# Kernel tuning notes

Hardware: AMD Instinct MI355X
Metric: run time of the kernel (lower is better)

The kernel has to match this reference:

```python
import jax, jax.numpy as jnp
import numpy as np

# ---- static config (mirrors init_kwargs and the chosen batch geometry) ----
HID = 4096; NH = 32; NKV = 8; HD = HID // NH; GRP = NH // NKV
PAGE = 16; MAXP = 2048; B = 4; QLEN = 512; PREV = 1016
THETA = 10000.0
PREV_PAGES = (PREV + PAGE - 1) // PAGE              # 64 pages already in cache per request
LAST_LEN = PREV - (PREV_PAGES - 1) * PAGE           # 8 valid slots in last cached page
NEW_PAGES = (QLEN + LAST_LEN + PAGE - 1) // PAGE - 1  # 32 pages allocated per request
TOT_PAGES = PREV_PAGES + NEW_PAGES                   # 96
KV_LEN = TOT_PAGES * PAGE                            # 1536 (padded)
TOT = PREV + QLEN                                    # 1528 valid kv tokens


def setup_inputs() -> dict:
    key = jax.random.key(0)
    ks = jax.random.split(key, 6)
    hidden_states = jax.random.normal(ks[0], (B, QLEN, HID), jnp.float32)
    paged_kv_data = jax.random.normal(ks[1], (MAXP, 2, PAGE, NKV, HD), jnp.float32)
    Wq = jax.random.normal(ks[2], (HID, HID), jnp.float32) * 0.02
    Wk = jax.random.normal(ks[3], (NKV * HD, HID), jnp.float32) * 0.02
    Wv = jax.random.normal(ks[4], (NKV * HD, HID), jnp.float32) * 0.02
    Wo = jax.random.normal(ks[5], (HID, HID), jnp.float32) * 0.02
    qo_indptr = jnp.arange(B + 1, dtype=jnp.int32) * QLEN
    paged_kv_indptr = jnp.arange(B + 1, dtype=jnp.int32) * PREV_PAGES
    paged_kv_indices = jnp.arange(B * PREV_PAGES, dtype=jnp.int32)  # pages 0..255 in use
    paged_kv_last_page_len = jnp.full((B,), LAST_LEN, jnp.int32)
    return dict(hidden_states=hidden_states, paged_kv_data=paged_kv_data,
                Wq=Wq, Wk=Wk, Wv=Wv, Wo=Wo, qo_indptr=qo_indptr,
                paged_kv_indptr=paged_kv_indptr, paged_kv_indices=paged_kv_indices,
                paged_kv_last_page_len=paged_kv_last_page_len)


def _rope(x, pos):
    # x: [B, L, H, D], pos: [L]; Llama rotate-half RoPE (flashinfer ROPE_LLAMA)
    d = x.shape[-1]; d2 = d // 2
    inv = 1.0 / (THETA ** (jnp.arange(0, d, 2, dtype=jnp.float32) / d))
    ang = pos[:, None] * inv                     # [L, d/2]
    cos = jnp.cos(ang)[None, :, None, :]
    sin = jnp.sin(ang)[None, :, None, :]
    x1, x2 = x[..., :d2], x[..., d2:]
    return jnp.concatenate([x1 * cos - x2 * sin, x2 * cos + x1 * sin], axis=-1)


def reference(hidden_states, paged_kv_data, Wq, Wk, Wv, Wo, qo_indptr,
              paged_kv_indptr, paged_kv_indices, paged_kv_last_page_len):
    q = (hidden_states @ Wq.T).reshape(B, QLEN, NH, HD)
    k = (hidden_states @ Wk.T).reshape(B, QLEN, NKV, HD)
    v = (hidden_states @ Wv.T).reshape(B, QLEN, NKV, HD)

    # ---- paged KV-cache append (vectorized form of update_kv_cache) ----
    # free pages in ascending id order, as in the torch mask/arange logic
    used = jnp.zeros((MAXP,), bool).at[paged_kv_indices].set(True)
    avail = jnp.sort(jnp.where(used, MAXP, jnp.arange(MAXP)))[: B * NEW_PAGES].astype(jnp.int32)
    new_pages = avail.reshape(B, NEW_PAGES)               # sequential per-request allocation
    last_page = paged_kv_indices[paged_kv_indptr[1:] - 1]  # [B] partially-filled last page
    append_pages = jnp.concatenate([last_page[:, None], new_pages], axis=1)  # [B, NEW_PAGES+1]
    t = LAST_LEN + jnp.arange(QLEN)                       # slot offset within the append window
    slot = t % PAGE                                       # [QLEN]
    dest_page = append_pages[:, t // PAGE]                # [B, QLEN]
    paged_kv_data = paged_kv_data.at[dest_page, 0, slot[None, :]].set(k)
    paged_kv_data = paged_kv_data.at[dest_page, 1, slot[None, :]].set(v)

    new_indices2d = jnp.concatenate([paged_kv_indices.reshape(B, PREV_PAGES), new_pages], axis=1)
    new_indptr = jnp.arange(B + 1, dtype=jnp.int32) * TOT_PAGES
    new_last = jnp.full((B,), (LAST_LEN + QLEN - 1) % PAGE + 1, jnp.int32)

    # ---- batched prefill attention over paged cache, RoPE applied on the fly ----
    K = paged_kv_data[new_indices2d, 0].reshape(B, KV_LEN, NKV, HD)
    V = paged_kv_data[new_indices2d, 1].reshape(B, KV_LEN, NKV, HD)
    kpos = jnp.arange(KV_LEN, dtype=jnp.float32)
    qpos = jnp.arange(PREV, PREV + QLEN, dtype=jnp.float32)
    qr = _rope(q, qpos)
    Kr = _rope(K, kpos)
    Kg = jnp.repeat(Kr, GRP, axis=2)   # GQA: each kv head serves GRP query heads
    Vg = jnp.repeat(V, GRP, axis=2)
    scores = jnp.einsum('bqhd,bkhd->bhqk', qr, Kg) * (HD ** -0.5)
    mask = (kpos[None, :] <= qpos[:, None]) & (kpos[None, :] < TOT)  # causal + padded-slot mask
    scores = jnp.where(mask[None, None], scores, jnp.float32(-1e30))
    attn = jax.nn.softmax(scores, axis=-1)
    out = jnp.einsum('bhqk,bkhd->bqhd', attn, Vg).reshape(B, QLEN, HID)
    out = out @ Wo.T
    return out, paged_kv_data, new_indptr, new_indices2d.reshape(-1), new_last
```

## Files before the change

### kernel.cpp

```cpp
#include <hip/hip_runtime.h>
#include <stdint.h>

#define B_ 4
#define QLEN_ 512
#define HID_ 4096
#define NH_ 32
#define NKV_ 8
#define HD_ 128
#define PREV_ 1016
#define TOTLEN_ 1528
#define KVLEN_ 1536
#define PREV_PAGES_ 64
#define NEW_PAGES_ 32
#define TOT_PAGES_ 96
#define MAXP_ 2048

typedef unsigned short u16;
typedef __attribute__((ext_vector_type(8))) short short8;
typedef __attribute__((ext_vector_type(4))) float f32x4;

__device__ __forceinline__ u16 f2bf(float x) {
  unsigned u = __float_as_uint(x);
  u += 0x7fffu + ((u >> 16) & 1u);
  return (u16)(u >> 16);
}

__global__ void conv_bf16(const float* __restrict__ in, u16* __restrict__ out, int n8) {
  int i = blockIdx.x * 256 + threadIdx.x;
  if (i >= n8) return;
  size_t base = (size_t)i * 8;
  float4 a = *(const float4*)(in + base);
  float4 b = *(const float4*)(in + base + 4);
  union { u16 u[8]; short8 v; } r;
  r.u[0] = f2bf(a.x); r.u[1] = f2bf(a.y); r.u[2] = f2bf(a.z); r.u[3] = f2bf(a.w);
  r.u[4] = f2bf(b.x); r.u[5] = f2bf(b.y); r.u[6] = f2bf(b.z); r.u[7] = f2bf(b.w);
  *(short8*)(out + base) = r.v;
}

__global__ void page_setup(const int* __restrict__ kv_indptr, const int* __restrict__ kv_indices,
                           float* __restrict__ out_ints, int* __restrict__ aps) {
  __shared__ unsigned char used[MAXP_];
  __shared__ int offs[256];
  __shared__ int avail[B_ * NEW_PAGES_];
  int tid = threadIdx.x;
  for (int j = tid; j < MAXP_; j += 256) used[j] = 0;
  __syncthreads();
  for (int j = tid; j < B_ * PREV_PAGES_; j += 256) used[kv_indices[j]] = 1;
  __syncthreads();
  int cnt = 0;
  for (int i = 0; i < 8; i++) cnt += 1 - (int)used[tid * 8 + i];
  offs[tid] = cnt;
  __syncthreads();
  if (tid == 0) {
    int run = 0;
    for (int i = 0; i < 256; i++) { int c = offs[i]; offs[i] = run; run += c; }
  }
  __syncthreads();
  int run = offs[tid];
  for (int i = 0; i < 8; i++) {
    int p = tid * 8 + i;
    if (!used[p]) { if (run < B_ * NEW_PAGES_) avail[run] = p; run++; }
  }
  __syncthreads();
  if (tid < B_ + 1) out_ints[tid] = (float)(tid * TOT_PAGES_);
  if (tid < B_) out_ints[B_ + 1 + B_ * TOT_PAGES_ + tid] = 8.0f;
  for (int j = tid; j < B_ * TOT_PAGES_; j += 256) {
    int b = j / TOT_PAGES_, r = j % TOT_PAGES_;
    int v = (r < PREV_PAGES_) ? kv_indices[b * PREV_PAGES_ + r] : avail[b * NEW_PAGES_ + (r - PREV_PAGES_)];
    out_ints[B_ + 1 + j] = (float)v;
  }
  for (int j = tid; j < B_ * 33; j += 256) {
    int b = j / 33, r = j % 33;
    aps[j] = (r == 0) ? kv_indices[kv_indptr[b + 1] - 1] : avail[b * NEW_PAGES_ + r - 1];
  }
}

__device__ __forceinline__ void async16(const u16* g, u16* l) {
  __builtin_amdgcn_global_load_lds((const __attribute__((address_space(1))) unsigned int*)g,
                                   (__attribute__((address_space(3))) unsigned int*)l, 16, 0, 0);
}

__global__ __launch_bounds__(256) void gemm_bt(const u16* __restrict__ A, const u16* __restrict__ Bm,
                                               float* __restrict__ C, int M, int N, int K) {
  __shared__ u16 a_sm[4096];
  __shared__ u16 b_sm[4096];
  const int tid = threadIdx.x;
  const int wave = tid >> 6, lane = tid & 63;
  const int quad = lane >> 4, l16 = lane & 15;
  const int wm = wave & 1, wn = wave >> 1;
  const size_t row0 = (size_t)blockIdx.y * 128, col0 = (size_t)blockIdx.x * 128;

  f32x4 zero4 = {0.f, 0.f, 0.f, 0.f};
  f32x4 acc[4][4];
#pragma unroll
  for (int i = 0; i < 4; i++)
#pragma unroll
    for (int j = 0; j < 4; j++) acc[i][j] = zero4;

  size_t aoffs[2], boffs[2];
  u16 *albase[2], *blbase[2];
#pragma unroll
  for (int i = 0; i < 2; i++) {
    int p = wave + i * 4;
    int c = p * 64 + lane;
    int r = c >> 2;
    int q = (c & 3) ^ ((r >> 1) & 3);
    aoffs[i] = (row0 + r) * (size_t)K + q * 8;
    boffs[i] = (col0 + r) * (size_t)K + q * 8;
    albase[i] = a_sm + p * 512;
    blbase[i] = b_sm + p * 512;
  }

  for (int k0 = 0; k0 < K; k0 += 32) {
    __syncthreads();
#pragma unroll
    for (int i = 0; i < 2; i++) {
      async16(A + aoffs[i] + k0, albase[i]);
      async16(Bm + boffs[i] + k0, blbase[i]);
    }
    __syncthreads();
    short8 af[4];
#pragma unroll
    for (int mt = 0; mt < 4; mt++) {
      int row = wm * 64 + mt * 16 + l16;
      int idx = row * 4 + (quad ^ ((row >> 1) & 3));
      af[mt] = *(const short8*)&a_sm[idx * 8];
    }
#pragma unroll
    for (int nt = 0; nt < 4; nt++) {
      int col = wn * 64 + nt * 16 + l16;
      int idx = col * 4 + (quad ^ ((col >> 1) & 3));
      short8 bf = *(const short8*)&b_sm[idx * 8];
#pragma unroll
      for (int mt = 0; mt < 4; mt++)
        acc[mt][nt] = __builtin_amdgcn_mfma_f32_16x16x32_bf16(af[mt], bf, acc[mt][nt], 0, 0, 0);
    }
  }
#pragma unroll
  for (int mt = 0; mt < 4; mt++)
#pragma unroll
    for (int nt = 0; nt < 4; nt++) {
      size_t col = col0 + wn * 64 + nt * 16 + l16;
#pragma unroll
      for (int r = 0; r < 4; r++) {
        size_t row = row0 + wm * 64 + mt * 16 + quad * 4 + r;
        C[row * N + col] = acc[mt][nt][r];
      }
    }
}

__global__ void scatter_kv(const float* __restrict__ kf, const float* __restrict__ vf,
                           const int* __restrict__ aps, float* __restrict__ outp) {
  int idx = blockIdx.x * 256 + threadIdx.x;
  int which = idx >> 19;
  int e4 = idx & 524287;
  size_t e = (size_t)e4 * 4;
  int bt = (int)(e >> 10);
  int b = bt >> 9, t = bt & 511;
  int c = (int)(e & 1023);
  int page = aps[b * 33 + ((8 + t) >> 4)];
  int slot = (8 + t) & 15;
  const float* src = which ? vf : kf;
  size_t dst = (((size_t)page * 2 + which) * 16 + slot) * 1024 + c;
  *(float4*)(outp + dst) = *(const float4*)(src + e);
}

__global__ void build_kc(const float* __restrict__ paged, const float* __restrict__ kf,
                         const int* __restrict__ kv_indices, u16* __restrict__ Kc) {
  int gid = blockIdx.x * 256 + threadIdx.x;
  int d2 = gid & 63;
  int rest = gid >> 6;
  int kpos = rest % KVLEN_;
  int bh = rest / KVLEN_;
  float x1 = 0.f, x2 = 0.f;
  if (kpos < PREV_) {
    int page = kv_indices[(bh >> 3) * PREV_PAGES_ + (kpos >> 4)];
    size_t base = (((size_t)page * 2) * 16 + (kpos & 15)) * 1024 + (bh & 7) * 128;
    x1 = paged[base + d2]; x2 = paged[base + d2 + 64];
  } else if (kpos < TOTLEN_) {
    size_t base = ((size_t)(bh >> 3) * 512 + (kpos - PREV_)) * 1024 + (bh & 7) * 128;
    x1 = kf[base + d2]; x2 = kf[base + d2 + 64];
  }
  float inv = exp2f((float)d2 * -0.20762050593046014f);
  float ang = (float)kpos * inv;
  float s, c;
  sincosf(ang, &s, &c);
  size_t ob = ((size_t)bh * KVLEN_ + kpos) * 128;
  Kc[ob + d2] = f2bf(x1 * c - x2 * s);
  Kc[ob + d2 + 64] = f2bf(x2 * c + x1 * s);
}

__global__ void build_vt(const float* __restrict__ paged, const float* __restrict__ vf,
                         const int* __restrict__ kv_indices, u16* __restrict__ Vt) {
  __shared__ float tile[64][129];
  int bx = blockIdx.x;
  int tk = bx % 24;
  int bh = bx / 24;
  int tid = threadIdx.x;
  for (int i = 0; i < 32; i++) {
    int e = tid + i * 256;
    int r = e >> 7, d = e & 127;
    int kpos = tk * 64 + r;
    float val = 0.f;
    if (kpos < PREV_) {
      int page = kv_indices[(bh >> 3) * PREV_PAGES_ + (kpos >> 4)];
      val = paged[(((size_t)page * 2 + 1) * 16 + (kpos & 15)) * 1024 + (bh & 7) * 128 + d];
    } else if (kpos < TOTLEN_) {
      val = vf[((size_t)(bh >> 3) * 512 + (kpos - PREV_)) * 1024 + (bh & 7) * 128 + d];
    }
    tile[r][d] = val;
  }
  __syncthreads();
  for (int i = 0; i < 32; i++) {
    int e = tid + i * 256;
    int d = e >> 6, kp = e & 63;
    Vt[((size_t)bh * 128 + d) * KVLEN_ + tk * 64 + kp] = f2bf(tile[kp][d]);
  }
}

__global__ void rope_q(const float* __restrict__ qf, u16* __restrict__ Qr) {
  int gid = blockIdx.x * 256 + threadIdx.x;
  int d2 = gid & 63;
  int t = (gid >> 6) & 511;
  int h = (gid >> 15) & 31;
  int b = gid >> 20;
  size_t base = ((size_t)(b * 512 + t)) * 4096 + h * 128;
  float x1 = qf[base + d2], x2 = qf[base + d2 + 64];
  float inv = exp2f((float)d2 * -0.20762050593046014f);
  float ang = (float)(PREV_ + t) * inv;
  float s, c;
  sincosf(ang, &s, &c);
  const float scale = 0.08838834764831845f;
  size_t ob = (((size_t)(b * 32 + h)) * 512 + t) * 128;
  Qr[ob + d2] = f2bf((x1 * c - x2 * s) * scale);
  Qr[ob + d2 + 64] = f2bf((x2 * c + x1 * s) * scale);
}

__global__ __launch_bounds__(256) void flash_attn(const u16* __restrict__ Qr, const u16* __restrict__ Kc,
                                                  const u16* __restrict__ Vt, u16* __restrict__ Obuf) {
  __shared__ u16 q_sm[64 * 136];
  __shared__ u16 k_sm[64 * 136];
  __shared__ u16 v_sm[128 * 72];
  __shared__ u16 p_sm[4 * 16 * 72];
  const int qb = blockIdx.x, h = blockIdx.y, b = blockIdx.z;
  const int kvh = h >> 2;
  const int tid = threadIdx.x, wave = tid >> 6, lane = tid & 63;
  const int quad = lane >> 4, l16 = lane & 15;

  const u16* Qbase = Qr + (((size_t)(b * 32 + h)) * 512 + qb * 64) * 128;
#pragma unroll
  for (int i = 0; i < 4; i++) {
    int c = tid + i * 256;
    int r = c >> 4, col = (c & 15) * 8;
    *(short8*)&q_sm[r * 136 + col] = *(const short8*)&Qbase[r * 128 + col];
  }
  __syncthreads();
  short8 aq[4];
#pragma unroll
  for (int kc = 0; kc < 4; kc++)
    aq[kc] = *(const short8*)&q_sm[(wave * 16 + l16) * 136 + kc * 32 + quad * 8];

  float m_i[4], l_i[4];
  f32x4 zero4 = {0.f, 0.f, 0.f, 0.f};
  f32x4 o_acc[8];
#pragma unroll
  for (int r = 0; r < 4; r++) { m_i[r] = -1e30f; l_i[r] = 0.f; }
#pragma unroll
  for (int dt = 0; dt < 8; dt++) o_acc[dt] = zero4;

  const u16* Kbase = Kc + ((size_t)(b * 8 + kvh)) * KVLEN_ * 128;
  const u16* Vbase = Vt + ((size_t)(b * 8 + kvh)) * 128 * KVLEN_;
  const int qlo = PREV_ + qb * 64;
  const int ntiles = (qlo + 63) / 64 + 1;

  for (int t = 0; t < ntiles; t++) {
    const int kb = t * 64;
    __syncthreads();
#pragma unroll
    for (int i = 0; i < 4; i++) {
      int c = tid + i * 256;
      {
        int r = c >> 4, col = (c & 15) * 8;
        *(short8*)&k_sm[r * 136 + col] = *(const short8*)&Kbase[(size_t)(kb + r) * 128 + col];
      }
      {
        int d = c >> 3, kcol = (c & 7) * 8;
        *(short8*)&v_sm[d * 72 + kcol] = *(const short8*)&Vbase[(size_t)d * KVLEN_ + kb + kcol];
      }
    }
    __syncthreads();
    f32x4 s[4];
#pragma unroll
    for (int nt = 0; nt < 4; nt++) {
      f32x4 acc = zero4;
#pragma unroll
      for (int kc = 0; kc < 4; kc++) {
        short8 bk = *(const short8*)&k_sm[(nt * 16 + l16) * 136 + kc * 32 + quad * 8];
        acc = __builtin_amdgcn_mfma_f32_16x16x32_bf16(aq[kc], bk, acc, 0, 0, 0);
      }
      s[nt] = acc;
    }
    if (kb + 63 > qlo + wave * 16 || kb + 63 >= TOTLEN_) {
#pragma unroll
      for (int nt = 0; nt < 4; nt++)
#pragma unroll
        for (int r = 0; r < 4; r++) {
          int kvcol = kb + nt * 16 + l16;
          int qp = qlo + wave * 16 + quad * 4 + r;
          if (kvcol > qp || kvcol >= TOTLEN_) s[nt][r] = -1e30f;
        }
    }
    float cur[4];
#pragma unroll
    for (int r = 0; r < 4; r++)
      cur[r] = fmaxf(fmaxf(s[0][r], s[1][r]), fmaxf(s[2][r], s[3][r]));
#pragma unroll
    for (int off = 1; off < 16; off <<= 1)
#pragma unroll
      for (int r = 0; r < 4; r++) cur[r] = fmaxf(cur[r], __shfl_xor(cur[r], off, 64));
    float alpha[4];
#pragma unroll
    for (int r = 0; r < 4; r++) {
      float mn = fmaxf(m_i[r], cur[r]);
      alpha[r] = __expf(m_i[r] - mn);
      m_i[r] = mn;
    }
#pragma unroll
    for (int nt = 0; nt < 4; nt++)
#pragma unroll
      for (int r = 0; r < 4; r++) s[nt][r] = __expf(s[nt][r] - m_i[r]);
    float rs[4];
#pragma unroll
    for (int r = 0; r < 4; r++) rs[r] = s[0][r] + s[1][r] + s[2][r] + s[3][r];
#pragma unroll
    for (int off = 1; off < 16; off <<= 1)
#pragma unroll
      for (int r = 0; r < 4; r++) rs[r] += __shfl_xor(rs[r], off, 64);
#pragma unroll
    for (int r = 0; r < 4; r++) l_i[r] = alpha[r] * l_i[r] + rs[r];
#pragma unroll
    for (int dt = 0; dt < 8; dt++)
#pragma unroll
      for (int r = 0; r < 4; r++) o_acc[dt][r] *= alpha[r];
#pragma unroll
    for (int nt = 0; nt < 4; nt++)
#pragma unroll
      for (int r = 0; r < 4; r++)
        p_sm[wave * 1152 + (quad * 4 + r) * 72 + nt * 16 + l16] = f2bf(s[nt][r]);
    __syncthreads();
#pragma unroll
    for (int kc = 0; kc < 2; kc++) {
      short8 ap = *(const short8*)&p_sm[wave * 1152 + l16 * 72 + kc * 32 + quad * 8];
#pragma unroll
      for (int dt = 0; dt < 8; dt++) {
        short8 bv = *(const short8*)&v_sm[(dt * 16 + l16) * 72 + kc * 32 + quad * 8];
        o_acc[dt] = __builtin_amdgcn_mfma_f32_16x16x32_bf16(ap, bv, o_acc[dt], 0, 0, 0);
      }
    }
  }
  size_t orow = ((size_t)(b * 512 + qb * 64 + wave * 16 + quad * 4)) * 4096 + (size_t)h * 128;
#pragma unroll
  for (int r = 0; r < 4; r++) {
    float invl = 1.f / l_i[r];
#pragma unroll
    for (int dt = 0; dt < 8; dt++)
      Obuf[orow + (size_t)r * 4096 + dt * 16 + l16] = f2bf(o_acc[dt][r] * invl);
  }
}

extern "C" void kernel_launch(void* const* d_in, const int* in_sizes, int n_in,
                              void* d_out, int out_size, void* d_ws, size_t ws_size,
                              hipStream_t stream) {
  const float* hidden = (const float*)d_in[0];
  const float* paged = (const float*)d_in[1];
  const float* Wq = (const float*)d_in[2];
  const float* Wk = (const float*)d_in[3];
  const float* Wv = (const float*)d_in[4];
  const float* Wo = (const float*)d_in[5];
  const int* kv_indptr = (const int*)d_in[7];
  const int* kv_indices = (const int*)d_in[8];

  float* out = (float*)d_out;
  float* out_paged = out + (size_t)B_ * QLEN_ * HID_;
  float* out_ints = out_paged + (size_t)MAXP_ * 2 * 16 * NKV_ * HD_;

  char* w = (char*)d_ws;
  u16* hid_bf = (u16*)(w + 0);
  u16* wq_bf = (u16*)(w + 16777216);
  u16* wk_bf = (u16*)(w + 50331648);
  u16* wv_bf = (u16*)(w + 58720256);
  u16* wo_bf = (u16*)(w + 67108864);
  float* q_f32 = (float*)(w + 100663296);
  float* k_f32 = (float*)(w + 134217728);
  float* v_f32 = (float*)(w + 142606336);
  u16* qr = (u16*)(w + 150994944);
  u16* kc = (u16*)(w + 167772160);
  u16* vt = (u16*)(w + 180355072);
  u16* obuf = (u16*)(w + 192937984);
  int* aps = (int*)(w + 209715200);

  hipMemcpyAsync(out_paged, paged, (size_t)MAXP_ * 2 * 16 * NKV_ * HD_ * 4,
                 hipMemcpyDeviceToDevice, stream);
  page_setup<<<1, 256, 0, stream>>>(kv_indptr, kv_indices, out_ints, aps);

  conv_bf16<<<4096, 256, 0, stream>>>(hidden, hid_bf, 8388608 / 8);
  conv_bf16<<<8192, 256, 0, stream>>>(Wq, wq_bf, 16777216 / 8);
  conv_bf16<<<2048, 256, 0, stream>>>(Wk, wk_bf, 4194304 / 8);
  conv_bf16<<<2048, 256, 0, stream>>>(Wv, wv_bf, 4194304 / 8);
  conv_bf16<<<8192, 256, 0, stream>>>(Wo, wo_bf, 16777216 / 8);

  gemm_bt<<<dim3(32, 16), 256, 0, stream>>>(hid_bf, wq_bf, q_f32, 2048, 4096, 4096);
  gemm_bt<<<dim3(8, 16), 256, 0, stream>>>(hid_bf, wk_bf, k_f32, 2048, 1024, 4096);
  gemm_bt<<<dim3(8, 16), 256, 0, stream>>>(hid_bf, wv_bf, v_f32, 2048, 1024, 4096);

  scatter_kv<<<4096, 256, 0, stream>>>(k_f32, v_f32, aps, out_paged);
  build_kc<<<12288, 256, 0, stream>>>(paged, k_f32, kv_indices, kc);
  build_vt<<<768, 256, 0, stream>>>(paged, v_f32, kv_indices, vt);
  rope_q<<<16384, 256, 0, stream>>>(q_f32, qr);

  flash_attn<<<dim3(8, 32, 4), 256, 0, stream>>>(qr, kc, vt, obuf);

  gemm_bt<<<dim3(32, 16), 256, 0, stream>>>(obuf, wo_bf, out, 2048, 4096, 4096);
}
```

Baseline: 1.212 ms.

## Fuse K/V projection GEMMs, fuse Q RoPE into attention, restructure softmax with transposed MFMA

The separate K and V projection GEMMs become one GEMM into an interleaved KV buffer, which relies on wk_bf and wv_bf sitting contiguously in the workspace. The rope_q kernel is removed and RoPE plus scaling is applied to Q inside flash_attn as it loads. The attention loop swaps MFMA operands so each lane owns one query row. That removes cross-lane shuffles and the P-buffer barrier, skips the rescale when the running max is unchanged, packs to bf16 with a single instruction, and adds s_setprio hints and coalesced output stores through LDS. The risks are that the Q RoPE work is now repeated per block and that occupancy hints may constrain registers.

```diff
diff --git a/kernel.cpp b/kernel.cpp
--- a/kernel.cpp
+++ b/kernel.cpp
@@ -25,6 +25,12 @@
   return (u16)(u >> 16);
 }
 
+__device__ __forceinline__ unsigned cvt_pk_bf16(float lo, float hi) {
+  unsigned r;
+  asm("v_cvt_pk_bf16_f32 %0, %1, %2" : "=v"(r) : "v"(lo), "v"(hi));
+  return r;
+}
+
 __global__ void conv_bf16(const float* __restrict__ in, u16* __restrict__ out, int n8) {
   int i = blockIdx.x * 256 + threadIdx.x;
   if (i >= n8) return;
@@ -149,8 +155,8 @@
     }
 }
 
-__global__ void scatter_kv(const float* __restrict__ kf, const float* __restrict__ vf,
-                           const int* __restrict__ aps, float* __restrict__ outp) {
+__global__ void scatter_kv(const float* __restrict__ kvf, const int* __restrict__ aps,
+                           float* __restrict__ outp) {
   int idx = blockIdx.x * 256 + threadIdx.x;
   int which = idx >> 19;
   int e4 = idx & 524287;
@@ -160,12 +166,12 @@
   int c = (int)(e & 1023);
   int page = aps[b * 33 + ((8 + t) >> 4)];
   int slot = (8 + t) & 15;
-  const float* src = which ? vf : kf;
   size_t dst = (((size_t)page * 2 + which) * 16 + slot) * 1024 + c;
-  *(float4*)(outp + dst) = *(const float4*)(src + e);
-}
-
-__global__ void build_kc(const float* __restrict__ paged, const float* __restrict__ kf,
+  size_t src = (size_t)bt * 2048 + which * 1024 + c;
+  *(float4*)(outp + dst) = *(const float4*)(kvf + src);
+}
+
+__global__ void build_kc(const float* __restrict__ paged, const float* __restrict__ kvf,
                          const int* __restrict__ kv_indices, u16* __restrict__ Kc) {
   int gid = blockIdx.x * 256 + threadIdx.x;
   int d2 = gid & 63;
@@ -178,8 +184,8 @@
     size_t base = (((size_t)page * 2) * 16 + (kpos & 15)) * 1024 + (bh & 7) * 128;
     x1 = paged[base + d2]; x2 = paged[base + d2 + 64];
   } else if (kpos < TOTLEN_) {
-    size_t base = ((size_t)(bh >> 3) * 512 + (kpos - PREV_)) * 1024 + (bh & 7) * 128;
-    x1 = kf[base + d2]; x2 = kf[base + d2 + 64];
+    size_t base = ((size_t)(bh >> 3) * 512 + (kpos - PREV_)) * 2048 + (bh & 7) * 128;
+    x1 = kvf[base + d2]; x2 = kvf[base + d2 + 64];
   }
   float inv = exp2f((float)d2 * -0.20762050593046014f);
   float ang = (float)kpos * inv;
@@ -190,7 +196,7 @@
   Kc[ob + d2 + 64] = f2bf(x2 * c + x1 * s);
 }
 
-__global__ void build_vt(const float* __restrict__ paged, const float* __restrict__ vf,
+__global__ void build_vt(const float* __restrict__ paged, const float* __restrict__ kvf,
                          const int* __restrict__ kv_indices, u16* __restrict__ Vt) {
   __shared__ float tile[64][129];
   int bx = blockIdx.x;
@@ -206,7 +212,7 @@
       int page = kv_indices[(bh >> 3) * PREV_PAGES_ + (kpos >> 4)];
       val = paged[(((size_t)page * 2 + 1) * 16 + (kpos & 15)) * 1024 + (bh & 7) * 128 + d];
     } else if (kpos < TOTLEN_) {
-      val = vf[((size_t)(bh >> 3) * 512 + (kpos - PREV_)) * 1024 + (bh & 7) * 128 + d];
+      val = kvf[((size_t)(bh >> 3) * 512 + (kpos - PREV_)) * 2048 + 1024 + (bh & 7) * 128 + d];
     }
     tile[r][d] = val;
   }
@@ -218,60 +224,50 @@
   }
 }
 
-__global__ void rope_q(const float* __restrict__ qf, u16* __restrict__ Qr) {
-  int gid = blockIdx.x * 256 + threadIdx.x;
-  int d2 = gid & 63;
-  int t = (gid >> 6) & 511;
-  int h = (gid >> 15) & 31;
-  int b = gid >> 20;
-  size_t base = ((size_t)(b * 512 + t)) * 4096 + h * 128;
-  float x1 = qf[base + d2], x2 = qf[base + d2 + 64];
-  float inv = exp2f((float)d2 * -0.20762050593046014f);
-  float ang = (float)(PREV_ + t) * inv;
-  float s, c;
-  sincosf(ang, &s, &c);
-  const float scale = 0.08838834764831845f;
-  size_t ob = (((size_t)(b * 32 + h)) * 512 + t) * 128;
-  Qr[ob + d2] = f2bf((x1 * c - x2 * s) * scale);
-  Qr[ob + d2 + 64] = f2bf((x2 * c + x1 * s) * scale);
-}
-
-__global__ __launch_bounds__(256) void flash_attn(const u16* __restrict__ Qr, const u16* __restrict__ Kc,
-                                                  const u16* __restrict__ Vt, u16* __restrict__ Obuf) {
-  __shared__ u16 q_sm[64 * 136];
+__global__ __launch_bounds__(256, 3) void flash_attn(const float* __restrict__ qf, const u16* __restrict__ Kc,
+                                                     const u16* __restrict__ Vt, u16* __restrict__ Obuf) {
+  __shared__ u16 qp_sm[64 * 136];
   __shared__ u16 k_sm[64 * 136];
   __shared__ u16 v_sm[128 * 72];
-  __shared__ u16 p_sm[4 * 16 * 72];
   const int qb = blockIdx.x, h = blockIdx.y, b = blockIdx.z;
   const int kvh = h >> 2;
   const int tid = threadIdx.x, wave = tid >> 6, lane = tid & 63;
   const int quad = lane >> 4, l16 = lane & 15;
 
-  const u16* Qbase = Qr + (((size_t)(b * 32 + h)) * 512 + qb * 64) * 128;
-#pragma unroll
-  for (int i = 0; i < 4; i++) {
-    int c = tid + i * 256;
-    int r = c >> 4, col = (c & 15) * 8;
-    *(short8*)&q_sm[r * 136 + col] = *(const short8*)&Qbase[r * 128 + col];
+  {
+    const float scale = 0.08838834764831845f;
+#pragma unroll
+    for (int i = 0; i < 16; i++) {
+      int e = i * 256 + tid;
+      int r = e >> 6, d2 = e & 63;
+      size_t base = ((size_t)(b * 512 + qb * 64 + r)) * 4096 + h * 128;
+      float x1 = qf[base + d2], x2 = qf[base + d2 + 64];
+      float inv = exp2f((float)d2 * -0.20762050593046014f);
+      float ang = (float)(PREV_ + qb * 64 + r) * inv;
+      float s, c;
+      sincosf(ang, &s, &c);
+      qp_sm[r * 136 + d2] = f2bf((x1 * c - x2 * s) * scale);
+      qp_sm[r * 136 + d2 + 64] = f2bf((x2 * c + x1 * s) * scale);
+    }
   }
   __syncthreads();
   short8 aq[4];
 #pragma unroll
   for (int kc = 0; kc < 4; kc++)
-    aq[kc] = *(const short8*)&q_sm[(wave * 16 + l16) * 136 + kc * 32 + quad * 8];
-
-  float m_i[4], l_i[4];
+    aq[kc] = *(const short8*)&qp_sm[(wave * 16 + l16) * 136 + kc * 32 + quad * 8];
+
+  float m_i = -1e30f, l_i = 0.f;
   f32x4 zero4 = {0.f, 0.f, 0.f, 0.f};
   f32x4 o_acc[8];
-#pragma unroll
-  for (int r = 0; r < 4; r++) { m_i[r] = -1e30f; l_i[r] = 0.f; }
 #pragma unroll
   for (int dt = 0; dt < 8; dt++) o_acc[dt] = zero4;
 
   const u16* Kbase = Kc + ((size_t)(b * 8 + kvh)) * KVLEN_ * 128;
   const u16* Vbase = Vt + ((size_t)(b * 8 + kvh)) * 128 * KVLEN_;
   const int qlo = PREV_ + qb * 64;
+  const int qpos = qlo + wave * 16 + l16;
   const int ntiles = (qlo + 63) / 64 + 1;
+  u16* prow = &qp_sm[(wave * 16 + l16) * 136];
 
   for (int t = 0; t < ntiles; t++) {
     const int kb = t * 64;
@@ -290,81 +286,94 @@
     }
     __syncthreads();
     f32x4 s[4];
+    __builtin_amdgcn_s_setprio(1);
 #pragma unroll
     for (int nt = 0; nt < 4; nt++) {
       f32x4 acc = zero4;
 #pragma unroll
       for (int kc = 0; kc < 4; kc++) {
         short8 bk = *(const short8*)&k_sm[(nt * 16 + l16) * 136 + kc * 32 + quad * 8];
-        acc = __builtin_amdgcn_mfma_f32_16x16x32_bf16(aq[kc], bk, acc, 0, 0, 0);
+        acc = __builtin_amdgcn_mfma_f32_16x16x32_bf16(bk, aq[kc], acc, 0, 0, 0);
       }
       s[nt] = acc;
     }
+    __builtin_amdgcn_s_setprio(0);
     if (kb + 63 > qlo + wave * 16 || kb + 63 >= TOTLEN_) {
 #pragma unroll
       for (int nt = 0; nt < 4; nt++)
 #pragma unroll
         for (int r = 0; r < 4; r++) {
-          int kvcol = kb + nt * 16 + l16;
-          int qp = qlo + wave * 16 + quad * 4 + r;
-          if (kvcol > qp || kvcol >= TOTLEN_) s[nt][r] = -1e30f;
+          int kv = kb + nt * 16 + quad * 4 + r;
+          if (kv > qpos || kv >= TOTLEN_) s[nt][r] = -1e30f;
         }
     }
-    float cur[4];
-#pragma unroll
-    for (int r = 0; r < 4; r++)
-      cur[r] = fmaxf(fmaxf(s[0][r], s[1][r]), fmaxf(s[2][r], s[3][r]));
-#pragma unroll
-    for (int off = 1; off < 16; off <<= 1)
-#pragma unroll
-      for (int r = 0; r < 4; r++) cur[r] = fmaxf(cur[r], __shfl_xor(cur[r], off, 64));
-    float alpha[4];
-#pragma unroll
-    for (int r = 0; r < 4; r++) {
-      float mn = fmaxf(m_i[r], cur[r]);
-      alpha[r] = __expf(m_i[r] - mn);
-      m_i[r] = mn;
-    }
-#pragma unroll
-    for (int nt = 0; nt < 4; nt++)
-#pragma unroll
-      for (int r = 0; r < 4; r++) s[nt][r] = __expf(s[nt][r] - m_i[r]);
-    float rs[4];
-#pragma unroll
-    for (int r = 0; r < 4; r++) rs[r] = s[0][r] + s[1][r] + s[2][r] + s[3][r];
-#pragma unroll
-    for (int off = 1; off < 16; off <<= 1)
-#pragma unroll
-      for (int r = 0; r < 4; r++) rs[r] += __shfl_xor(rs[r], off, 64);
-#pragma unroll
-    for (int r = 0; r < 4; r++) l_i[r] = alpha[r] * l_i[r] + rs[r];
-#pragma unroll
-    for (int dt = 0; dt < 8; dt++)
-#pragma unroll
-      for (int r = 0; r < 4; r++) o_acc[dt][r] *= alpha[r];
-#pragma unroll
-    for (int nt = 0; nt < 4; nt++)
-#pragma unroll
-      for (int r = 0; r < 4; r++)
-        p_sm[wave * 1152 + (quad * 4 + r) * 72 + nt * 16 + l16] = f2bf(s[nt][r]);
-    __syncthreads();
+    float cur = fmaxf(fmaxf(fmaxf(s[0][0], s[0][1]), fmaxf(s[0][2], s[0][3])),
+                      fmaxf(fmaxf(s[1][0], s[1][1]), fmaxf(s[1][2], s[1][3])));
+    cur = fmaxf(cur, fmaxf(fmaxf(fmaxf(s[2][0], s[2][1]), fmaxf(s[2][2], s[2][3])),
+                           fmaxf(fmaxf(s[3][0], s[3][1]), fmaxf(s[3][2], s[3][3]))));
+    cur = fmaxf(cur, __shfl_xor(cur, 16, 64));
+    cur = fmaxf(cur, __shfl_xor(cur, 32, 64));
+    if (!__all(cur <= m_i)) {
+      float mn = fmaxf(m_i, cur);
+      float alpha = __expf(m_i - mn);
+      m_i = mn;
+      l_i *= alpha;
+#pragma unroll
+      for (int dt = 0; dt < 8; dt++)
+#pragma unroll
+        for (int r = 0; r < 4; r++) o_acc[dt][r] *= alpha;
+    }
+    float psum = 0.f;
+    unsigned pk0[4], pk1[4];
+#pragma unroll
+    for (int nt = 0; nt < 4; nt++) {
+      float e0 = __expf(s[nt][0] - m_i);
+      float e1 = __expf(s[nt][1] - m_i);
+      float e2 = __expf(s[nt][2] - m_i);
+      float e3 = __expf(s[nt][3] - m_i);
+      psum += (e0 + e1) + (e2 + e3);
+      pk0[nt] = cvt_pk_bf16(e0, e1);
+      pk1[nt] = cvt_pk_bf16(e2, e3);
+    }
+    l_i += psum;
+#pragma unroll
+    for (int nt = 0; nt < 4; nt++) {
+      uint2 t2;
+      t2.x = pk0[nt];
+      t2.y = pk1[nt];
+      *(uint2*)&prow[nt * 16 + quad * 4] = t2;
+    }
+    __builtin_amdgcn_s_setprio(1);
 #pragma unroll
     for (int kc = 0; kc < 2; kc++) {
-      short8 ap = *(const short8*)&p_sm[wave * 1152 + l16 * 72 + kc * 32 + quad * 8];
+      short8 pfrag = *(const short8*)&prow[kc * 32 + quad * 8];
 #pragma unroll
       for (int dt = 0; dt < 8; dt++) {
-        short8 bv = *(const short8*)&v_sm[(dt * 16 + l16) * 72 + kc * 32 + quad * 8];
-        o_acc[dt] = __builtin_amdgcn_mfma_f32_16x16x32_bf16(ap, bv, o_acc[dt], 0, 0, 0);
+        short8 av = *(const short8*)&v_sm[(dt * 16 + l16) * 72 + kc * 32 + quad * 8];
+        o_acc[dt] = __builtin_amdgcn_mfma_f32_16x16x32_bf16(av, pfrag, o_acc[dt], 0, 0, 0);
       }
     }
-  }
-  size_t orow = ((size_t)(b * 512 + qb * 64 + wave * 16 + quad * 4)) * 4096 + (size_t)h * 128;
-#pragma unroll
-  for (int r = 0; r < 4; r++) {
-    float invl = 1.f / l_i[r];
-#pragma unroll
-    for (int dt = 0; dt < 8; dt++)
-      Obuf[orow + (size_t)r * 4096 + dt * 16 + l16] = f2bf(o_acc[dt][r] * invl);
+    __builtin_amdgcn_s_setprio(0);
+  }
+  l_i += __shfl_xor(l_i, 16, 64);
+  l_i += __shfl_xor(l_i, 32, 64);
+  float invl = 1.f / l_i;
+  __syncthreads();
+  u16* orow = &k_sm[(wave * 16 + l16) * 136];
+#pragma unroll
+  for (int dt = 0; dt < 8; dt++) {
+    uint2 t2;
+    t2.x = cvt_pk_bf16(o_acc[dt][0] * invl, o_acc[dt][1] * invl);
+    t2.y = cvt_pk_bf16(o_acc[dt][2] * invl, o_acc[dt][3] * invl);
+    *(uint2*)&orow[dt * 16 + quad * 4] = t2;
+  }
+  int rr = lane >> 2, cc = lane & 3;
+  const u16* srow = &k_sm[(wave * 16 + rr) * 136];
+  size_t gbase = ((size_t)(b * 512 + qb * 64 + wave * 16 + rr)) * 4096 + (size_t)h * 128;
+#pragma unroll
+  for (int i = 0; i < 4; i++) {
+    int col = (cc + i * 4) * 8;
+    *(short8*)&Obuf[gbase + col] = *(const short8*)&srow[col];
   }
 }
 
@@ -391,9 +400,7 @@
   u16* wv_bf = (u16*)(w + 58720256);
   u16* wo_bf = (u16*)(w + 67108864);
   float* q_f32 = (float*)(w + 100663296);
-  float* k_f32 = (float*)(w + 134217728);
-  float* v_f32 = (float*)(w + 142606336);
-  u16* qr = (u16*)(w + 150994944);
+  float* kv_f32 = (float*)(w + 134217728);
   u16* kc = (u16*)(w + 167772160);
   u16* vt = (u16*)(w + 180355072);
   u16* obuf = (u16*)(w + 192937984);
@@ -410,15 +417,13 @@
   conv_bf16<<<8192, 256, 0, stream>>>(Wo, wo_bf, 16777216 / 8);
 
   gemm_bt<<<dim3(32, 16), 256, 0, stream>>>(hid_bf, wq_bf, q_f32, 2048, 4096, 4096);
-  gemm_bt<<<dim3(8, 16), 256, 0, stream>>>(hid_bf, wk_bf, k_f32, 2048, 1024, 4096);
-  gemm_bt<<<dim3(8, 16), 256, 0, stream>>>(hid_bf, wv_bf, v_f32, 2048, 1024, 4096);
-
-  scatter_kv<<<4096, 256, 0, stream>>>(k_f32, v_f32, aps, out_paged);
-  build_kc<<<12288, 256, 0, stream>>>(paged, k_f32, kv_indices, kc);
-  build_vt<<<768, 256, 0, stream>>>(paged, v_f32, kv_indices, vt);
-  rope_q<<<16384, 256, 0, stream>>>(q_f32, qr);
-
-  flash_attn<<<dim3(8, 32, 4), 256, 0, stream>>>(qr, kc, vt, obuf);
+  gemm_bt<<<dim3(16, 16), 256, 0, stream>>>(hid_bf, wk_bf, kv_f32, 2048, 2048, 4096);
+
+  scatter_kv<<<4096, 256, 0, stream>>>(kv_f32, aps, out_paged);
+  build_kc<<<12288, 256, 0, stream>>>(paged, kv_f32, kv_indices, kc);
+  build_vt<<<768, 256, 0, stream>>>(paged, kv_f32, kv_indices, vt);
+
+  flash_attn<<<dim3(8, 32, 4), 256, 0, stream>>>(q_f32, kc, vt, obuf);
 
   gemm_bt<<<dim3(32, 16), 256, 0, stream>>>(obuf, wo_bf, out, 2048, 4096, 4096);
 }
```

Result: faster. 1.081 ms (-10.8%).
